# Optimization experiments

Measured on AMD Instinct MI355X. Metric: run time of the kernel, lower is better.

The kernel has to match this reference:

```python
import jax, jax.numpy as jnp
import numpy as np

N_NODES = 50000
N_EDGES = 1_250_000
D_FEAT = 64


def setup_inputs() -> dict:
    key = jax.random.key(0)
    k1, k2, k3 = jax.random.split(key, 3)
    graph_embedding = jax.random.normal(k1, (N_NODES, D_FEAT), dtype=jnp.float32)
    src = jax.random.randint(k2, (N_EDGES,), 0, N_NODES, dtype=jnp.int64)
    dst = jax.random.randint(k3, (N_EDGES,), 0, N_NODES, dtype=jnp.int64)
    return {"graph_embedding": graph_embedding, "src": src, "dst": dst}


def reference(graph_embedding, src, dst):
    # DGL update_all(copy_u('ft','m'), sum('m','ft')):
    # out[v] = sum over edges (u->v) of graph_embedding[u]
    messages = graph_embedding[src]  # [E, d] gather
    out = jax.ops.segment_sum(messages, dst, num_segments=graph_embedding.shape[0])
    return out
```

## Files before the change

kernel.cpp:

```cpp
#include <hip/hip_runtime.h>


#define D_FEAT 64
#define NB2    512
#define CAPB   3072
#define MAXNB  512
#define PCHUNK 8192
#define CAP1   96

static __device__ __forceinline__ unsigned short f2bf(float f) {
    unsigned u = __float_as_uint(f);
    u += 0x7fffu + ((u >> 16) & 1u);
    return (unsigned short)(u >> 16);
}

__global__ __launch_bounds__(512) void fused_cvt_partition_kernel(
    const float4* __restrict__ emb4,
    uint2*        __restrict__ embh2,
    const int*    __restrict__ src,
    const int*    __restrict__ dst,
    unsigned*     __restrict__ cursor,
    unsigned*     __restrict__ packed,
    int n4, int cvt_blocks, int n_edges, unsigned npb_inv)
{
    __shared__ unsigned lpk[PCHUNK];
    __shared__ unsigned lhist[MAXNB];
    __shared__ unsigned lbase[MAXNB];

    if ((int)blockIdx.x < cvt_blocks) {
        int i = blockIdx.x * 512 + threadIdx.x;
        if (i < n4) {
            float4 x = emb4[i];
            uint2 o;
            o.x = (unsigned)f2bf(x.x) | ((unsigned)f2bf(x.y) << 16);
            o.y = (unsigned)f2bf(x.z) | ((unsigned)f2bf(x.w) << 16);
            embh2[i] = o;
        }
        return;
    }

    int pb   = blockIdx.x - cvt_blocks;
    int t    = threadIdx.x;
    int base = pb * PCHUNK;
    int cnt  = n_edges - base; if (cnt > PCHUNK) cnt = PCHUNK; if (cnt < 0) cnt = 0;

    for (int i = t; i < MAXNB; i += 512) lhist[i] = 0;
    __syncthreads();

    int nv = cnt >> 2;
    const int4* d4 = (const int4*)(dst + base);
    const int4* s4 = (const int4*)(src + base);
    for (int i = t; i < nv; i += 512) {
        int4 d = d4[i];
        int4 s = s4[i];
        uint4 pkw;
        pkw.x = ((unsigned)d.x << 16) | (unsigned)s.x;
        pkw.y = ((unsigned)d.y << 16) | (unsigned)s.y;
        pkw.z = ((unsigned)d.z << 16) | (unsigned)s.z;
        pkw.w = ((unsigned)d.w << 16) | (unsigned)s.w;
        ((uint4*)lpk)[i] = pkw;
        atomicAdd(&lhist[__umulhi(pkw.x >> 16, npb_inv)], 1u);
        atomicAdd(&lhist[__umulhi(pkw.y >> 16, npb_inv)], 1u);
        atomicAdd(&lhist[__umulhi(pkw.z >> 16, npb_inv)], 1u);
        atomicAdd(&lhist[__umulhi(pkw.w >> 16, npb_inv)], 1u);
    }
    for (int i = nv * 4 + t; i < cnt; i += 512) {
        unsigned dd = (unsigned)dst[base + i];
        lpk[i] = (dd << 16) | (unsigned)src[base + i];
        atomicAdd(&lhist[__umulhi(dd, npb_inv)], 1u);
    }
    __syncthreads();

    for (int i = t; i < MAXNB; i += 512) {
        unsigned c = lhist[i];
        lbase[i] = c ? atomicAdd(&cursor[i], c) : 0u;
        lhist[i] = 0;
    }
    __syncthreads();

    for (int i = t; i < cnt; i += 512) {
        unsigned p = lpk[i];
        unsigned b = __umulhi(p >> 16, npb_inv);
        unsigned off = atomicAdd(&lhist[b], 1u);
        unsigned pos = lbase[b] + off;
        if (pos < CAPB)
            packed[(size_t)b * CAPB + pos] = p;
    }
}

#define ACC8(h) \
    a0 += __uint_as_float(h.x << 16);           \
    a1 += __uint_as_float(h.x & 0xffff0000u);   \
    a2 += __uint_as_float(h.y << 16);           \
    a3 += __uint_as_float(h.y & 0xffff0000u);   \
    a4 += __uint_as_float(h.z << 16);           \
    a5 += __uint_as_float(h.z & 0xffff0000u);   \
    a6 += __uint_as_float(h.w << 16);           \
    a7 += __uint_as_float(h.w & 0xffff0000u);

__global__ __launch_bounds__(1024, 8) void sortgather_kernel(
    const unsigned short* __restrict__ embh,
    const unsigned*       __restrict__ cursor,
    const unsigned*       __restrict__ packed,
    float*                __restrict__ out,
    int n_nodes, unsigned npb)
{
    __shared__ unsigned       lpk[CAPB];
    __shared__ unsigned short slist[CAPB];
    __shared__ unsigned       hist[128];
    __shared__ unsigned       cur[128];
    __shared__ unsigned       stc[128];

    int b = blockIdx.x;
    int t = threadIdx.x;
    int node_base = (int)(b * npb);
    int nn = n_nodes - node_base;
    if (nn > (int)npb) nn = (int)npb;
    if (nn < 0) nn = 0;

    int cnt = (int)cursor[b]; if (cnt > CAPB) cnt = CAPB;
    const unsigned* pk = packed + (size_t)b * CAPB;

    if (t < 128) hist[t] = 0;
    __syncthreads();

    for (int i = t; i < cnt; i += 1024) {
        unsigned p = pk[i];
        lpk[i] = p;
        atomicAdd(&hist[(p >> 16) - node_base], 1u);
    }
    __syncthreads();

    if (t < 64) {
        int l = t;
        unsigned v0 = hist[2 * l], v1 = hist[2 * l + 1];
        unsigned s = v0 + v1;
        unsigned inc = s;
        #pragma unroll
        for (int d = 1; d < 64; d <<= 1) {
            unsigned u = __shfl_up(inc, d);
            if (l >= d) inc += u;
        }
        unsigned exc = inc - s;
        cur[2 * l]     = exc;
        cur[2 * l + 1] = exc + v0;
        stc[2 * l]     = (exc << 16) | v0;
        stc[2 * l + 1] = ((exc + v0) << 16) | v1;
    }
    __syncthreads();

    for (int i = t; i < cnt; i += 1024) {
        unsigned p = lpk[i];
        unsigned pos = atomicAdd(&cur[(p >> 16) - node_base], 1u);
        slist[pos] = (unsigned short)(p & 0xffffu);
    }
    __syncthreads();

    int g  = t >> 3;
    int l8 = t & 7;

    unsigned sc = stc[g];
    int st = (int)(sc >> 16), cn = (int)(sc & 0xffffu);

    float a0=0.f,a1=0.f,a2=0.f,a3=0.f,a4=0.f,a5=0.f,a6=0.f,a7=0.f;

    for (int j = 0; j < cn; j += 8) {
        bool v1 = j + 1 < cn, v2 = j + 2 < cn, v3 = j + 3 < cn;
        bool v4 = j + 4 < cn, v5 = j + 5 < cn, v6 = j + 6 < cn, v7 = j + 7 < cn;
        uint4 h0, h1, h2, h3, h4, h5, h6, h7;
        h0 =          *(const uint4*)(embh + ((size_t)slist[st + j    ] << 6) + l8 * 8);
        if (v1) h1 =  *(const uint4*)(embh + ((size_t)slist[st + j + 1] << 6) + l8 * 8);
        if (v2) h2 =  *(const uint4*)(embh + ((size_t)slist[st + j + 2] << 6) + l8 * 8);
        if (v3) h3 =  *(const uint4*)(embh + ((size_t)slist[st + j + 3] << 6) + l8 * 8);
        if (v4) h4 =  *(const uint4*)(embh + ((size_t)slist[st + j + 4] << 6) + l8 * 8);
        if (v5) h5 =  *(const uint4*)(embh + ((size_t)slist[st + j + 5] << 6) + l8 * 8);
        if (v6) h6 =  *(const uint4*)(embh + ((size_t)slist[st + j + 6] << 6) + l8 * 8);
        if (v7) h7 =  *(const uint4*)(embh + ((size_t)slist[st + j + 7] << 6) + l8 * 8);
        { ACC8(h0); }
        if (v1) { ACC8(h1); }
        if (v2) { ACC8(h2); }
        if (v3) { ACC8(h3); }
        if (v4) { ACC8(h4); }
        if (v5) { ACC8(h5); }
        if (v6) { ACC8(h6); }
        if (v7) { ACC8(h7); }
    }

    if (g < nn) {
        float4* o4 = (float4*)(out + (size_t)(node_base + g) * D_FEAT + l8 * 8);
        o4[0] = make_float4(a0, a1, a2, a3);
        o4[1] = make_float4(a4, a5, a6, a7);
    }
}

__global__ __launch_bounds__(256) void count_scatter_kernel(
    const int* __restrict__ src, const int* __restrict__ dst,
    int* __restrict__ cnt, int* __restrict__ bucket, int n_edges)
{
    int e = blockIdx.x * blockDim.x + threadIdx.x;
    if (e >= n_edges) return;
    int s = src[e], d = dst[e];
    int pos = atomicAdd(&cnt[d], 1);
    if (pos < CAP1) bucket[(size_t)d * CAP1 + pos] = s;
}

__global__ __launch_bounds__(256) void gather_sum_kernel(
    const float* __restrict__ emb, const int* __restrict__ cnt,
    const int* __restrict__ bucket, float* __restrict__ out, int n_nodes)
{
    int v = (blockIdx.x * blockDim.x + threadIdx.x) >> 6;
    int lane = threadIdx.x & 63;
    if (v >= n_nodes) return;
    int n = cnt[v]; if (n > CAP1) n = CAP1;
    const int* b = bucket + (size_t)v * CAP1;
    float acc = 0.f;
    for (int j = 0; j < n; ++j)
        acc += emb[(size_t)b[j] * D_FEAT + lane];
    out[(size_t)v * D_FEAT + lane] = acc;
}

__global__ __launch_bounds__(256) void scatter_sum_fallback(
    const float* __restrict__ emb, const int* __restrict__ src,
    const int* __restrict__ dst, float* __restrict__ out, int n_edges)
{
    int gid = blockIdx.x * blockDim.x + threadIdx.x;
    int e = gid >> 4;
    if (e >= n_edges) return;
    int c = gid & 15;
    int s = src[e], d = dst[e];
    const float4* emb4 = (const float4*)emb;
    float4 v = emb4[(size_t)s * 16 + c];
    float* o = out + (size_t)d * D_FEAT + c * 4;
    atomicAdd(o + 0, v.x); atomicAdd(o + 1, v.y);
    atomicAdd(o + 2, v.z); atomicAdd(o + 3, v.w);
}

extern "C" void kernel_launch(void* const* d_in, const int* in_sizes, int n_in,
                              void* d_out, int out_size, void* d_ws, size_t ws_size,
                              hipStream_t stream) {
    const float* emb = (const float*)d_in[0];
    const int*   src = (const int*)d_in[1];
    const int*   dst = (const int*)d_in[2];
    float*       out = (float*)d_out;

    int n_edges = in_sizes[1];
    int n_nodes = out_size / D_FEAT;

    unsigned npb = (unsigned)((n_nodes + NB2 - 1) / NB2);
    if (npb == 0) npb = 1;
    int nb = (n_nodes + (int)npb - 1) / (int)npb;
    unsigned npb_inv = (unsigned)((0x100000000ULL + npb - 1) / npb);

    size_t cur_b  = 4096;
    size_t pack_b = (size_t)MAXNB * CAPB * sizeof(unsigned);
    size_t embh_b = (size_t)n_nodes * D_FEAT * sizeof(unsigned short);

    if (n_nodes <= 65536 && npb <= 128 && nb <= MAXNB &&
        ws_size >= cur_b + pack_b + embh_b) {
        char* p = (char*)d_ws;
        unsigned*       cursor = (unsigned*)p;        p += cur_b;
        unsigned*       packed = (unsigned*)p;        p += pack_b;
        unsigned short* embh   = (unsigned short*)p;

        hipMemsetAsync(cursor, 0, (size_t)MAXNB * sizeof(unsigned), stream);

        int n4 = n_nodes * D_FEAT / 4;
        int cvt_blocks = (n4 + 511) / 512;
        int p_blocks   = (n_edges + PCHUNK - 1) / PCHUNK;
        fused_cvt_partition_kernel<<<cvt_blocks + p_blocks, 512, 0, stream>>>(
            (const float4*)emb, (uint2*)embh, src, dst, cursor, packed,
            n4, cvt_blocks, n_edges, npb_inv);

        sortgather_kernel<<<nb, 1024, 0, stream>>>(
            embh, cursor, packed, out, n_nodes, npb);
    } else if (ws_size >= (size_t)n_nodes * sizeof(int) * (1 + CAP1)) {
        int* cnt    = (int*)d_ws;
        int* bucket = (int*)((char*)d_ws + (size_t)n_nodes * sizeof(int));
        hipMemsetAsync(cnt, 0, (size_t)n_nodes * sizeof(int), stream);
        count_scatter_kernel<<<(n_edges + 255) / 256, 256, 0, stream>>>(
            src, dst, cnt, bucket, n_edges);
        gather_sum_kernel<<<(n_nodes * 64 + 255) / 256, 256, 0, stream>>>(
            emb, cnt, bucket, out, n_nodes);
    } else {
        hipMemsetAsync(d_out, 0, (size_t)out_size * sizeof(float), stream);
        long long total = (long long)n_edges * 16;
        scatter_sum_fallback<<<(int)((total + 255) / 256), 256, 0, stream>>>(
            emb, src, dst, out, n_edges);
    }
}
```

Before: 104.9 us.

## Keep partition edges in registers, drop LDS staging, use 1024-thread blocks

The partition phase now uses 1024-thread blocks, and each thread holds its two int4 groups of packed edges in registers instead of staging the whole 8192-edge chunk in a 32 KB shared array. This cuts LDS footprint and the re-read of shared memory in the scatter pass, which should raise occupancy. Partition blocks are now placed before conversion blocks so the heavier work is scheduled first. Each conversion block now handles four float4s per thread, so fewer blocks are launched. Register-held edges assume nv is at most 2048, which holds for PCHUNK 8192; the tail path reloads src and dst from global memory.

```diff
diff --git a/kernel.cpp b/kernel.cpp
--- a/kernel.cpp
+++ b/kernel.cpp
@@ -14,78 +14,97 @@
     return (unsigned short)(u >> 16);
 }
 
-__global__ __launch_bounds__(512) void fused_cvt_partition_kernel(
+__global__ __launch_bounds__(1024) void fused_cvt_partition_kernel(
     const float4* __restrict__ emb4,
     uint2*        __restrict__ embh2,
     const int*    __restrict__ src,
     const int*    __restrict__ dst,
     unsigned*     __restrict__ cursor,
     unsigned*     __restrict__ packed,
-    int n4, int cvt_blocks, int n_edges, unsigned npb_inv)
-{
-    __shared__ unsigned lpk[PCHUNK];
+    int n4, int p_blocks, int n_edges, unsigned npb_inv)
+{
     __shared__ unsigned lhist[MAXNB];
     __shared__ unsigned lbase[MAXNB];
 
-    if ((int)blockIdx.x < cvt_blocks) {
-        int i = blockIdx.x * 512 + threadIdx.x;
-        if (i < n4) {
-            float4 x = emb4[i];
-            uint2 o;
-            o.x = (unsigned)f2bf(x.x) | ((unsigned)f2bf(x.y) << 16);
-            o.y = (unsigned)f2bf(x.z) | ((unsigned)f2bf(x.w) << 16);
-            embh2[i] = o;
+    if ((int)blockIdx.x >= p_blocks) {
+        int cb = blockIdx.x - p_blocks;
+        int base = cb * 4096 + (int)threadIdx.x;
+        #pragma unroll
+        for (int r = 0; r < 4; ++r) {
+            int i = base + r * 1024;
+            if (i < n4) {
+                float4 x = emb4[i];
+                uint2 o;
+                o.x = (unsigned)f2bf(x.x) | ((unsigned)f2bf(x.y) << 16);
+                o.y = (unsigned)f2bf(x.z) | ((unsigned)f2bf(x.w) << 16);
+                embh2[i] = o;
+            }
         }
         return;
     }
 
-    int pb   = blockIdx.x - cvt_blocks;
+    int pb   = blockIdx.x;
     int t    = threadIdx.x;
     int base = pb * PCHUNK;
     int cnt  = n_edges - base; if (cnt > PCHUNK) cnt = PCHUNK; if (cnt < 0) cnt = 0;
 
-    for (int i = t; i < MAXNB; i += 512) lhist[i] = 0;
+    for (int i = t; i < MAXNB; i += 1024) lhist[i] = 0;
     __syncthreads();
 
     int nv = cnt >> 2;
     const int4* d4 = (const int4*)(dst + base);
     const int4* s4 = (const int4*)(src + base);
-    for (int i = t; i < nv; i += 512) {
-        int4 d = d4[i];
-        int4 s = s4[i];
-        uint4 pkw;
-        pkw.x = ((unsigned)d.x << 16) | (unsigned)s.x;
-        pkw.y = ((unsigned)d.y << 16) | (unsigned)s.y;
-        pkw.z = ((unsigned)d.z << 16) | (unsigned)s.z;
-        pkw.w = ((unsigned)d.w << 16) | (unsigned)s.w;
-        ((uint4*)lpk)[i] = pkw;
-        atomicAdd(&lhist[__umulhi(pkw.x >> 16, npb_inv)], 1u);
-        atomicAdd(&lhist[__umulhi(pkw.y >> 16, npb_inv)], 1u);
-        atomicAdd(&lhist[__umulhi(pkw.z >> 16, npb_inv)], 1u);
-        atomicAdd(&lhist[__umulhi(pkw.w >> 16, npb_inv)], 1u);
-    }
-    for (int i = nv * 4 + t; i < cnt; i += 512) {
-        unsigned dd = (unsigned)dst[base + i];
-        lpk[i] = (dd << 16) | (unsigned)src[base + i];
-        atomicAdd(&lhist[__umulhi(dd, npb_inv)], 1u);
-    }
-    __syncthreads();
-
-    for (int i = t; i < MAXNB; i += 512) {
+    int  i0 = t, i1 = t + 1024;
+    bool f0 = i0 < nv, f1 = i1 < nv;
+    uint4 pa, pb4;
+    if (f0) {
+        int4 d = d4[i0]; int4 s = s4[i0];
+        pa.x = ((unsigned)d.x << 16) | (unsigned)s.x;
+        pa.y = ((unsigned)d.y << 16) | (unsigned)s.y;
+        pa.z = ((unsigned)d.z << 16) | (unsigned)s.z;
+        pa.w = ((unsigned)d.w << 16) | (unsigned)s.w;
+    }
+    if (f1) {
+        int4 d = d4[i1]; int4 s = s4[i1];
+        pb4.x = ((unsigned)d.x << 16) | (unsigned)s.x;
+        pb4.y = ((unsigned)d.y << 16) | (unsigned)s.y;
+        pb4.z = ((unsigned)d.z << 16) | (unsigned)s.z;
+        pb4.w = ((unsigned)d.w << 16) | (unsigned)s.w;
+    }
+    if (f0) {
+        atomicAdd(&lhist[__umulhi(pa.x >> 16, npb_inv)], 1u);
+        atomicAdd(&lhist[__umulhi(pa.y >> 16, npb_inv)], 1u);
+        atomicAdd(&lhist[__umulhi(pa.z >> 16, npb_inv)], 1u);
+        atomicAdd(&lhist[__umulhi(pa.w >> 16, npb_inv)], 1u);
+    }
+    if (f1) {
+        atomicAdd(&lhist[__umulhi(pb4.x >> 16, npb_inv)], 1u);
+        atomicAdd(&lhist[__umulhi(pb4.y >> 16, npb_inv)], 1u);
+        atomicAdd(&lhist[__umulhi(pb4.z >> 16, npb_inv)], 1u);
+        atomicAdd(&lhist[__umulhi(pb4.w >> 16, npb_inv)], 1u);
+    }
+    for (int i = nv * 4 + t; i < cnt; i += 1024)
+        atomicAdd(&lhist[__umulhi((unsigned)dst[base + i], npb_inv)], 1u);
+    __syncthreads();
+
+    for (int i = t; i < MAXNB; i += 1024) {
         unsigned c = lhist[i];
         lbase[i] = c ? atomicAdd(&cursor[i], c) : 0u;
         lhist[i] = 0;
     }
     __syncthreads();
 
-    for (int i = t; i < cnt; i += 512) {
-        unsigned p = lpk[i];
-        unsigned b = __umulhi(p >> 16, npb_inv);
-        unsigned off = atomicAdd(&lhist[b], 1u);
-        unsigned pos = lbase[b] + off;
-        if (pos < CAPB)
-            packed[(size_t)b * CAPB + pos] = p;
-    }
+    #define SCAT(p) { \
+        unsigned b_ = __umulhi((p) >> 16, npb_inv); \
+        unsigned pos_ = lbase[b_] + atomicAdd(&lhist[b_], 1u); \
+        if (pos_ < CAPB) packed[(size_t)b_ * CAPB + pos_] = (p); }
+    if (f0) { SCAT(pa.x); SCAT(pa.y); SCAT(pa.z); SCAT(pa.w); }
+    if (f1) { SCAT(pb4.x); SCAT(pb4.y); SCAT(pb4.z); SCAT(pb4.w); }
+    for (int i = nv * 4 + t; i < cnt; i += 1024) {
+        unsigned p = ((unsigned)dst[base + i] << 16) | (unsigned)src[base + i];
+        SCAT(p);
+    }
+    #undef SCAT
 }
 
 #define ACC8(h) \
@@ -265,11 +284,11 @@
         hipMemsetAsync(cursor, 0, (size_t)MAXNB * sizeof(unsigned), stream);
 
         int n4 = n_nodes * D_FEAT / 4;
-        int cvt_blocks = (n4 + 511) / 512;
         int p_blocks   = (n_edges + PCHUNK - 1) / PCHUNK;
-        fused_cvt_partition_kernel<<<cvt_blocks + p_blocks, 512, 0, stream>>>(
+        int cvt_blocks = (n4 + 4095) / 4096;
+        fused_cvt_partition_kernel<<<p_blocks + cvt_blocks, 1024, 0, stream>>>(
             (const float4*)emb, (uint2*)embh, src, dst, cursor, packed,
-            n4, cvt_blocks, n_edges, npb_inv);
+            n4, p_blocks, n_edges, npb_inv);
 
         sortgather_kernel<<<nb, 1024, 0, stream>>>(
             embh, cursor, packed, out, n_nodes, npb);
```

Measured after the change: 100.8 us, median of 2. 1.04x faster.
